# Performance work log

Hardware: AMD Instinct MI355X
Metric: run time of the kernel (lower is better)

Reference implementation:

```python
import jax, jax.numpy as jnp
import numpy as np

MIN_KEEP = 0.1  # min_keep_ratio
MAX_KEEP = 1.0


def setup_inputs() -> dict:
    key = jax.random.key(0)
    k1, k2, k3, k4 = jax.random.split(key, 4)
    B, T, C = 8, 4096, 2048
    hidden = jax.random.normal(k1, (B, T, C), dtype=jnp.float32)
    keep_ratio = jax.random.uniform(k2, (B,), dtype=jnp.float32)
    W = jax.random.normal(k3, (C,), dtype=jnp.float32) * (1.0 / np.sqrt(C))
    b = jax.random.normal(k4, (1,), dtype=jnp.float32)
    return {"hidden": hidden, "keep_ratio": keep_ratio, "W": W, "b": b}


def reference(hidden, keep_ratio, W, b):
    # scores: [B, T] = Linear(dim, 1) projection, squeezed
    scores = jnp.einsum("btc,c->bt", hidden, W) + b[0]
    T = scores.shape[1]
    kr = jnp.clip(keep_ratio, MIN_KEEP, MAX_KEEP)          # [B]
    # k = max(1, int(kr * T)); int() truncates toward zero (kr*T >= 0)
    k = jnp.maximum(1, (kr * T).astype(jnp.int32))         # [B]
    # Batched variable-k top-k via rank: rank[b, t] = position of token t
    # in descending score order; token kept iff rank < k[b].
    order = jnp.argsort(-scores, axis=1)                   # [B, T] descending
    rank = jnp.argsort(order, axis=1)                      # [B, T]
    token_mask = rank < k[:, None]                         # [B, T] bool
    return token_mask, scores
```

## Files before the change

### kernel.cpp

```cpp
#include <hip/hip_runtime.h>

#define C_DIM 2048
#define T_TOKENS 4096

typedef float v4f __attribute__((ext_vector_type(4)));

__global__ __launch_bounds__(256) void score_kernel(
    const float* __restrict__ hidden, const float* __restrict__ W,
    const float* __restrict__ bptr, float* __restrict__ scores, int n_tokens) {
  const int wave = (int)((blockIdx.x * blockDim.x + threadIdx.x) >> 6);
  const int lane = threadIdx.x & 63;
  if (wave >= n_tokens) return;
  const float* row = hidden + (size_t)wave * C_DIM;
  double ax = 0.0, ay = 0.0, az = 0.0, aw = 0.0;
#pragma unroll
  for (int it = 0; it < C_DIM / (64 * 4); ++it) {
    const int c = it * 256 + lane * 4;
    v4f h = __builtin_nontemporal_load(reinterpret_cast<const v4f*>(row + c));
    v4f w = *reinterpret_cast<const v4f*>(W + c);
    ax += (double)h.x * (double)w.x;
    ay += (double)h.y * (double)w.y;
    az += (double)h.z * (double)w.z;
    aw += (double)h.w * (double)w.w;
  }
  double acc = (ax + ay) + (az + aw);
  for (int o = 32; o; o >>= 1) acc += __shfl_xor(acc, o);
  if (lane == 0) scores[wave] = (float)(acc + (double)bptr[0]);
}

__global__ __launch_bounds__(256) void topk_mask_kernel(
    const float* __restrict__ keep_ratio, const float* __restrict__ scores_all,
    float* __restrict__ mask) {
  const int b = blockIdx.x;
  const float* scores = scores_all + (size_t)b * T_TOKENS;
  __shared__ int s_hist[256];
  __shared__ int s_wave[4];
  __shared__ unsigned int s_sel;
  __shared__ int s_krem;
  const int tid = threadIdx.x;
  const int lane = tid & 63;
  const int wv = tid >> 6;

  float kf = fminf(fmaxf(keep_ratio[b], 0.1f), 1.0f);
  int k = (int)(kf * (float)T_TOKENS);
  if (k < 1) k = 1;

  unsigned int key[16];
  const float* base = scores + tid * 16;
#pragma unroll
  for (int i = 0; i < 16; i += 4) {
    float4 s4 = *reinterpret_cast<const float4*>(base + i);
    float ss[4] = {s4.x, s4.y, s4.z, s4.w};
#pragma unroll
    for (int j = 0; j < 4; ++j) {
      unsigned int u = __float_as_uint(ss[j]);
      key[i + j] = (u & 0x80000000u) ? ~u : (u | 0x80000000u);
    }
  }

  unsigned int prefix = 0u;
  int krem = k;
#pragma unroll
  for (int round = 0; round < 4; ++round) {
    const int shift = 24 - 8 * round;
    const unsigned int pmask = (round == 0) ? 0u : (0xFFFFFFFFu << (shift + 8));

    s_hist[tid] = 0;
    __syncthreads();
#pragma unroll
    for (int i = 0; i < 16; ++i) {
      if ((key[i] & pmask) == prefix)
        atomicAdd(&s_hist[(key[i] >> shift) & 255], 1);
    }
    __syncthreads();

    int v = s_hist[tid];
    int x = v;
#pragma unroll
    for (int off = 1; off < 64; off <<= 1) {
      int y = __shfl_down(x, off);
      if (lane + off < 64) x += y;
    }
    if (lane == 0) s_wave[wv] = x;
    __syncthreads();
    int add = 0;
    for (int w = wv + 1; w < 4; ++w) add += s_wave[w];
    const int suffix_incl = x + add;
    const int suffix_excl = suffix_incl - v;
    if (suffix_excl < krem && suffix_incl >= krem) {
      s_sel = (unsigned int)tid;
      s_krem = krem - suffix_excl;
    }
    __syncthreads();
    prefix |= (s_sel << shift);
    krem = s_krem;
    __syncthreads();
  }

  int cnt = 0;
#pragma unroll
  for (int i = 0; i < 16; ++i) cnt += (key[i] == prefix) ? 1 : 0;
  int inc = cnt;
#pragma unroll
  for (int off = 1; off < 64; off <<= 1) {
    int y = __shfl_up(inc, off);
    if (lane >= off) inc += y;
  }
  if (lane == 63) s_wave[wv] = inc;
  __syncthreads();
  int waveoff = 0;
  for (int w = 0; w < wv; ++w) waveoff += s_wave[w];
  int run = waveoff + inc - cnt;

  float* mrow = mask + (size_t)b * T_TOKENS + tid * 16;
#pragma unroll
  for (int i = 0; i < 16; i += 4) {
    float4 m4;
    float mv[4];
#pragma unroll
    for (int j = 0; j < 4; ++j) {
      unsigned int kk = key[i + j];
      bool keep = (kk > prefix) || (kk == prefix && run < krem);
      run += (kk == prefix) ? 1 : 0;
      mv[j] = keep ? 1.0f : 0.0f;
    }
    m4.x = mv[0]; m4.y = mv[1]; m4.z = mv[2]; m4.w = mv[3];
    *reinterpret_cast<float4*>(mrow + i) = m4;
  }
}

extern "C" void kernel_launch(void* const* d_in, const int* in_sizes, int n_in,
                              void* d_out, int out_size, void* d_ws, size_t ws_size,
                              hipStream_t stream) {
  const float* hidden = (const float*)d_in[0];
  const float* keep_ratio = (const float*)d_in[1];
  const float* W = (const float*)d_in[2];
  const float* bptr = (const float*)d_in[3];

  const int B = in_sizes[1];
  const int n_tokens = in_sizes[0] / C_DIM;

  float* out = (float*)d_out;
  float* mask = out;
  float* scores = out + (size_t)n_tokens;

  const int blocks = (n_tokens + 3) / 4;
  score_kernel<<<blocks, 256, 0, stream>>>(hidden, W, bptr, scores, n_tokens);
  topk_mask_kernel<<<B, 256, 0, stream>>>(keep_ratio, scores, mask);
}
```

Measured before the change: 49.10 us.

## Use 1024-thread blocks and 3-round 11-bit radix select in top-k mask kernel

The top-k mask kernel now runs 1024 threads per batch row, each holding 4 keys instead of 16. The radix select drops from four 8-bit rounds to three rounds of 11/11/10 bits with a 2048-bin shared histogram, and each thread scans two bins. This cuts per-thread serial work and the number of barrier-separated rounds in a kernel that only launches B=8 blocks. In exchange it adds a larger histogram to clear and a 16-wave cross-wave suffix sum.

```diff
diff --git a/kernel.cpp b/kernel.cpp
--- a/kernel.cpp
+++ b/kernel.cpp
@@ -28,13 +28,13 @@
   if (lane == 0) scores[wave] = (float)(acc + (double)bptr[0]);
 }
 
-__global__ __launch_bounds__(256) void topk_mask_kernel(
+__global__ __launch_bounds__(1024) void topk_mask_kernel(
     const float* __restrict__ keep_ratio, const float* __restrict__ scores_all,
     float* __restrict__ mask) {
   const int b = blockIdx.x;
   const float* scores = scores_all + (size_t)b * T_TOKENS;
-  __shared__ int s_hist[256];
-  __shared__ int s_wave[4];
+  __shared__ int s_hist[2048];
+  __shared__ int s_wtot[16];
   __shared__ unsigned int s_sel;
   __shared__ int s_krem;
   const int tid = threadIdx.x;
@@ -45,51 +45,62 @@
   int k = (int)(kf * (float)T_TOKENS);
   if (k < 1) k = 1;
 
-  unsigned int key[16];
-  const float* base = scores + tid * 16;
-#pragma unroll
-  for (int i = 0; i < 16; i += 4) {
-    float4 s4 = *reinterpret_cast<const float4*>(base + i);
+  unsigned int key[4];
+  {
+    float4 s4 = *reinterpret_cast<const float4*>(scores + tid * 4);
     float ss[4] = {s4.x, s4.y, s4.z, s4.w};
 #pragma unroll
     for (int j = 0; j < 4; ++j) {
       unsigned int u = __float_as_uint(ss[j]);
-      key[i + j] = (u & 0x80000000u) ? ~u : (u | 0x80000000u);
+      key[j] = (u & 0x80000000u) ? ~u : (u | 0x80000000u);
     }
   }
 
+  const int shifts[3] = {21, 10, 0};
+  const int nbins_arr[3] = {2048, 2048, 1024};
   unsigned int prefix = 0u;
   int krem = k;
 #pragma unroll
-  for (int round = 0; round < 4; ++round) {
-    const int shift = 24 - 8 * round;
-    const unsigned int pmask = (round == 0) ? 0u : (0xFFFFFFFFu << (shift + 8));
+  for (int round = 0; round < 3; ++round) {
+    const int shift = shifts[round];
+    const int nbins = nbins_arr[round];
+    const unsigned int bmask = (unsigned int)(nbins - 1);
+    const unsigned int pmask =
+        (round == 0) ? 0u : ~((1u << shifts[round - 1]) - 1u);
 
     s_hist[tid] = 0;
+    s_hist[tid + 1024] = 0;
     __syncthreads();
 #pragma unroll
-    for (int i = 0; i < 16; ++i) {
-      if ((key[i] & pmask) == prefix)
-        atomicAdd(&s_hist[(key[i] >> shift) & 255], 1);
+    for (int j = 0; j < 4; ++j) {
+      if ((key[j] & pmask) == prefix)
+        atomicAdd(&s_hist[(key[j] >> shift) & bmask], 1);
     }
     __syncthreads();
 
-    int v = s_hist[tid];
-    int x = v;
+    const int h0 = s_hist[2 * tid];
+    const int h1 = s_hist[2 * tid + 1];
+    int x = h0 + h1;
 #pragma unroll
     for (int off = 1; off < 64; off <<= 1) {
       int y = __shfl_down(x, off);
       if (lane + off < 64) x += y;
     }
-    if (lane == 0) s_wave[wv] = x;
+    if (lane == 0) s_wtot[wv] = x;
     __syncthreads();
     int add = 0;
-    for (int w = wv + 1; w < 4; ++w) add += s_wave[w];
-    const int suffix_incl = x + add;
-    const int suffix_excl = suffix_incl - v;
-    if (suffix_excl < krem && suffix_incl >= krem) {
-      s_sel = (unsigned int)tid;
-      s_krem = krem - suffix_excl;
+    for (int w = wv + 1; w < 16; ++w) add += s_wtot[w];
+    const int incl0 = x + add;
+    const int incl1 = incl0 - h0;
+    const int excl0 = incl1;
+    const int excl1 = incl1 - h1;
+    if (h0 > 0 && excl0 < krem && incl0 >= krem && 2 * tid < nbins) {
+      s_sel = (unsigned int)(2 * tid);
+      s_krem = krem - excl0;
+    }
+    if (h1 > 0 && excl1 < krem && incl1 >= krem && 2 * tid + 1 < nbins) {
+      s_sel = (unsigned int)(2 * tid + 1);
+      s_krem = krem - excl1;
     }
     __syncthreads();
     prefix |= (s_sel << shift);
@@ -99,34 +110,30 @@
 
   int cnt = 0;
 #pragma unroll
-  for (int i = 0; i < 16; ++i) cnt += (key[i] == prefix) ? 1 : 0;
+  for (int j = 0; j < 4; ++j) cnt += (key[j] == prefix) ? 1 : 0;
   int inc = cnt;
 #pragma unroll
   for (int off = 1; off < 64; off <<= 1) {
     int y = __shfl_up(inc, off);
     if (lane >= off) inc += y;
   }
-  if (lane == 63) s_wave[wv] = inc;
+  if (lane == 63) s_wtot[wv] = inc;
   __syncthreads();
   int waveoff = 0;
-  for (int w = 0; w < wv; ++w) waveoff += s_wave[w];
+  for (int w = 0; w < wv; ++w) waveoff += s_wtot[w];
   int run = waveoff + inc - cnt;
 
-  float* mrow = mask + (size_t)b * T_TOKENS + tid * 16;
+  float4 m4;
+  float mv[4];
 #pragma unroll
-  for (int i = 0; i < 16; i += 4) {
-    float4 m4;
-    float mv[4];
-#pragma unroll
-    for (int j = 0; j < 4; ++j) {
-      unsigned int kk = key[i + j];
-      bool keep = (kk > prefix) || (kk == prefix && run < krem);
-      run += (kk == prefix) ? 1 : 0;
-      mv[j] = keep ? 1.0f : 0.0f;
-    }
-    m4.x = mv[0]; m4.y = mv[1]; m4.z = mv[2]; m4.w = mv[3];
-    *reinterpret_cast<float4*>(mrow + i) = m4;
+  for (int j = 0; j < 4; ++j) {
+    unsigned int kk = key[j];
+    bool keep = (kk > prefix) || (kk == prefix && run < krem);
+    run += (kk == prefix) ? 1 : 0;
+    mv[j] = keep ? 1.0f : 0.0f;
   }
+  m4.x = mv[0]; m4.y = mv[1]; m4.z = mv[2]; m4.w = mv[3];
+  *reinterpret_cast<float4*>(mask + (size_t)b * T_TOKENS + tid * 4) = m4;
 }
 
 extern "C" void kernel_launch(void* const* d_in, const int* in_sizes, int n_in,
@@ -146,5 +153,5 @@
 
   const int blocks = (n_tokens + 3) / 4;
   score_kernel<<<blocks, 256, 0, stream>>>(hidden, W, bptr, scores, n_tokens);
-  topk_mask_kernel<<<B, 256, 0, stream>>>(keep_ratio, scores, mask);
+  topk_mask_kernel<<<B, 1024, 0, stream>>>(keep_ratio, scores, mask);
 }
```

Result: faster. 48.12 us (-2.0%).
